# Performance work log

Hardware: AMD Instinct MI355X
Metric: run time of the kernel (lower is better)

The kernel has to match this reference:

```python
import jax, jax.numpy as jnp
import numpy as np

ORDER = 32
ATAN_ALPHA = 2.0  # spikingjelly surrogate.ATan default


@jax.custom_vjp
def atan_spike(x):
    # Heaviside forward with ATan surrogate gradient (spikingjelly ATan)
    return (x >= 0).astype(x.dtype)

def _atan_fwd(x):
    return (x >= 0).astype(x.dtype), x

def _atan_bwd(x, g):
    s = (jnp.pi / 2.0) * ATAN_ALPHA * x
    return (g * (ATAN_ALPHA / 2.0) / (1.0 + s * s),)

atan_spike.defvjp(_atan_fwd, _atan_bwd)


def gen_gemm_weight(w, T):
    # W[i, j] = w[order-1 - (i-j)] if 0 <= i-j < order else 0 (banded lower Toeplitz)
    i = jnp.arange(T)[:, None]
    j = jnp.arange(T)[None, :]
    d = i - j
    idx = jnp.clip(ORDER - 1 - d, 0, ORDER - 1)
    return jnp.where((d >= 0) & (d < ORDER), w[idx], jnp.zeros((), w.dtype))


def setup_inputs() -> dict:
    key = jax.random.key(0)
    k1, = jax.random.split(key, 1)
    B, T, D = 16, 1024, 1024
    x_seq = jax.random.normal(k1, (B, T, D), dtype=jnp.float32)
    # exp_init: weight[order-1] = 1, weight[i] = weight[i+1] / 2
    weight = (2.0 ** jnp.arange(1 - ORDER, 1, dtype=jnp.float32))
    threshold = -jnp.ones((1,), dtype=jnp.float32)
    return {"x_seq": x_seq, "weight": weight, "threshold": threshold}


def reference(x_seq, weight, threshold):
    T = x_seq.shape[1]
    W = gen_gemm_weight(weight, T)                      # [T, T]
    # F.linear over the time axis: h[b,t,d] = sum_k W[t,k] x[b,k,d] + threshold
    h = jnp.einsum("tk,bkd->btd", W, x_seq) + threshold
    return atan_spike(h)
```

## Files before the change

kernel.cpp:

```cpp
#include <hip/hip_runtime.h>
#include <math.h>

#define ORDER 32
#define TC 32

__global__ __launch_bounds__(256)
void psn_kernel(const float* __restrict__ x,
                const float* __restrict__ w,
                const float* __restrict__ thr_p,
                float* __restrict__ out)
{
    const int T = 1024, D = 1024;
    const int d  = blockIdx.x * blockDim.x + threadIdx.x;
    const int t0 = blockIdx.y * TC;
    const int b  = blockIdx.z;

    __shared__ float ws[ORDER];
    if (threadIdx.x < ORDER) ws[threadIdx.x] = w[threadIdx.x];
    __syncthreads();

    const float thr = thr_p[0];
    const size_t base = (size_t)b * T * D + d;
    const float* xb = x + base;
    float*       ob = out + base;

    float xv[TC + ORDER - 1];
    if (t0 != 0) {
        const float* p = xb + (size_t)(t0 - (ORDER - 1)) * D;
        #pragma unroll
        for (int i = 0; i < TC + ORDER - 1; ++i)
            xv[i] = p[(size_t)i * D];
    } else {
        #pragma unroll
        for (int i = 0; i < TC + ORDER - 1; ++i) {
            const int t = i - (ORDER - 1);
            xv[i] = (t >= 0) ? xb[(size_t)t * D] : 0.0f;
        }
    }

    float wr[ORDER];
    #pragma unroll
    for (int j = 0; j < ORDER; ++j) wr[j] = ws[j];

    #pragma unroll
    for (int tt = 0; tt < TC; ++tt) {
        float h = thr;
        #pragma unroll
        for (int j = 0; j < ORDER; ++j)
            h = fmaf(wr[j], xv[tt + j], h);

        float res;
        if (__builtin_expect(fabsf(h) < 1e-3f, 0)) {
            double hd = (double)thr;
            #pragma unroll
            for (int j = 0; j < ORDER; ++j)
                hd = fma((double)wr[j], (double)xv[tt + j], hd);
            res = (hd >= 0.0) ? 1.0f : 0.0f;
        } else {
            res = (h >= 0.0f) ? 1.0f : 0.0f;
        }
        ob[(size_t)(t0 + tt) * D] = res;
    }
}

extern "C" void kernel_launch(void* const* d_in, const int* in_sizes, int n_in,
                              void* d_out, int out_size, void* d_ws, size_t ws_size,
                              hipStream_t stream)
{
    const float* x   = (const float*)d_in[0];
    const float* w   = (const float*)d_in[1];
    const float* thr = (const float*)d_in[2];
    float* o = (float*)d_out;

    dim3 grid(1024 / 256, 1024 / TC, 16);
    psn_kernel<<<grid, 256, 0, stream>>>(x, w, thr, o);
}
```

Measured before the change: 125.9 us.

## Stream input rows with prefetch distance instead of loading full window upfront

Replaces the upfront load of all 63 input rows with an initial load of ORDER-1+PF rows, then one row prefetched PF steps ahead inside the time loop. This lowers register pressure, which the new launch_bounds occupancy hint of 6 relies on to raise occupancy. Weights are now read straight from global (uniform, likely scalar loads) rather than staged through shared memory with a barrier. The catch is that memory latency is hidden only PF steps deep, so each load may stall if occupancy does not make up for it.

```diff
diff --git a/kernel.cpp b/kernel.cpp
--- a/kernel.cpp
+++ b/kernel.cpp
@@ -3,58 +3,49 @@
 
 #define ORDER 32
 #define TC 32
+#define PF 4
+#define WLEN (TC + ORDER - 1)
 
-__global__ __launch_bounds__(256)
+__global__ __launch_bounds__(256, 6)
 void psn_kernel(const float* __restrict__ x,
                 const float* __restrict__ w,
                 const float* __restrict__ thr_p,
                 float* __restrict__ out)
 {
-    const int T = 1024, D = 1024;
-    const int d  = blockIdx.x * blockDim.x + threadIdx.x;
+    const int D = 1024;
+    const int d  = blockIdx.x * 256 + threadIdx.x;
     const int t0 = blockIdx.y * TC;
     const int b  = blockIdx.z;
 
-    __shared__ float ws[ORDER];
-    if (threadIdx.x < ORDER) ws[threadIdx.x] = w[threadIdx.x];
-    __syncthreads();
-
     const float thr = thr_p[0];
-    const size_t base = (size_t)b * T * D + d;
+    const size_t base = (size_t)b * 1024 * D + d;
     const float* xb = x + base;
     float*       ob = out + base;
 
-    float xv[TC + ORDER - 1];
-    if (t0 != 0) {
-        const float* p = xb + (size_t)(t0 - (ORDER - 1)) * D;
-        #pragma unroll
-        for (int i = 0; i < TC + ORDER - 1; ++i)
-            xv[i] = p[(size_t)i * D];
-    } else {
-        #pragma unroll
-        for (int i = 0; i < TC + ORDER - 1; ++i) {
-            const int t = i - (ORDER - 1);
-            xv[i] = (t >= 0) ? xb[(size_t)t * D] : 0.0f;
-        }
+    float xv[WLEN];
+
+    #pragma unroll
+    for (int i = 0; i < ORDER - 1 + PF; ++i) {
+        const int t = t0 - (ORDER - 1) + i;
+        xv[i] = (t >= 0) ? xb[(size_t)t * D] : 0.0f;
     }
-
-    float wr[ORDER];
-    #pragma unroll
-    for (int j = 0; j < ORDER; ++j) wr[j] = ws[j];
 
     #pragma unroll
     for (int tt = 0; tt < TC; ++tt) {
+        if (ORDER - 1 + tt + PF < WLEN)
+            xv[ORDER - 1 + tt + PF] = xb[(size_t)(t0 + tt + PF) * D];
+
         float h = thr;
         #pragma unroll
         for (int j = 0; j < ORDER; ++j)
-            h = fmaf(wr[j], xv[tt + j], h);
+            h = fmaf(w[j], xv[tt + j], h);
 
         float res;
         if (__builtin_expect(fabsf(h) < 1e-3f, 0)) {
             double hd = (double)thr;
             #pragma unroll
             for (int j = 0; j < ORDER; ++j)
-                hd = fma((double)wr[j], (double)xv[tt + j], hd);
+                hd = fma((double)w[j], (double)xv[tt + j], hd);
             res = (hd >= 0.0) ? 1.0f : 0.0f;
         } else {
             res = (h >= 0.0f) ? 1.0f : 0.0f;
```

Result: slower. 218.2 us (+73.4%).
